# Kernel optimization log

Measured on AMD Instinct MI355X. Metric: run time of the kernel, lower is better.

## Reference

```python
import jax, jax.numpy as jnp
import numpy as np

B, C, H, W = 16, 384, 64, 64
S, R, GR = 16, 8, 64
EPS = 1e-6


def setup_inputs() -> dict:
    key = jax.random.key(0)
    ks = jax.random.split(key, 16)
    def rn(k, shape, s):
        return jax.random.normal(k, shape, dtype=jnp.float32) * s
    inp = {"x": jax.random.normal(ks[0], (B, C, H, W), dtype=jnp.float32)}
    i = 1
    for p in ("row", "col"):
        inp[p + "_a_logit"] = jnp.zeros((S,), jnp.float32)
        inp[p + "_U"] = rn(ks[i], (S, R), 0.02); i += 1
        inp[p + "_V"] = rn(ks[i], (S, R), 0.02); i += 1
        inp[p + "_Win"] = rn(ks[i], (S, C), 1.0 / np.sqrt(C)); i += 1
        inp[p + "_bin"] = jnp.zeros((S,), jnp.float32)
        inp[p + "_Wg"] = rn(ks[i], (S, C), 1.0 / np.sqrt(C)); i += 1
        inp[p + "_bg"] = jnp.zeros((S,), jnp.float32)
        inp[p + "_Wout"] = rn(ks[i], (C, S), 1.0 / np.sqrt(S)); i += 1
        inp[p + "_bout"] = jnp.zeros((C,), jnp.float32)
        inp[p + "_Wskip"] = rn(ks[i], (C, C), 1.0 / np.sqrt(C)); i += 1
        inp[p + "_bskip"] = jnp.zeros((C,), jnp.float32)
    inp["g1_w"] = rn(ks[i], (GR, C), 1.0 / np.sqrt(C)); i += 1
    inp["g1_b"] = jnp.zeros((GR,), jnp.float32)
    inp["g2_w"] = rn(ks[i], (C, GR), 1.0 / np.sqrt(GR)); i += 1
    inp["g2_b"] = jnp.zeros((C,), jnp.float32)
    inp["norm_w"] = jnp.ones((C,), jnp.float32)
    inp["norm_b"] = jnpp = jnp.zeros((C,), jnp.float32)
    inp["norm_b"] = jnp.zeros((C,), jnp.float32)
    return inp


def _ssm1d(x, a_logit, U, V, Win, bin_, Wg, bg, Wout, bout, Wskip, bskip, reverse):
    # x: [N, L, D]
    if reverse:
        x = x[:, ::-1]
    u = jnp.einsum('nld,sd->nls', x, Win) + bin_          # [N,L,S]
    g = jax.nn.sigmoid(jnp.einsum('nld,sd->nls', x, Wg) + bg)
    a = jax.nn.sigmoid(a_logit)                            # [S]
    # h_t = a*h + g_t*u_t + h @ (U V^T)^T  ==  h @ (diag(a) + (U V^T)^T) + g_t*u_t
    A = jnp.diag(a) + (U @ V.T).T                          # [S,S]
    gu = jnp.swapaxes(g * u, 0, 1)                         # [L,N,S]
    h0 = jnp.zeros((x.shape[0], a.shape[0]), x.dtype)

    def step(h, gu_t):
        h = h @ A + gu_t
        return h, h

    _, hs = jax.lax.scan(step, h0, gu)                     # [L,N,S]
    hs = jnp.swapaxes(hs, 0, 1)                            # [N,L,S]
    y = (jnp.einsum('nls,ds->nld', hs, Wout) + bout
         + jnp.einsum('nld,ed->nle', x, Wskip) + bskip)
    if reverse:
        y = y[:, ::-1]
    return y


def _forward(x, rp, cp, g1_w, g1_b, g2_w, g2_b, norm_w, norm_b):
    Bx, Cx, Hx, Wx = x.shape
    rows = jnp.transpose(x, (0, 2, 3, 1)).reshape(Bx * Hx, Wx, Cx)
    cols = jnp.transpose(x, (0, 3, 2, 1)).reshape(Bx * Wx, Hx, Cx)
    yr = _ssm1d(rows, *rp, False) + _ssm1d(rows, *rp, True)
    yc = _ssm1d(cols, *cp, False) + _ssm1d(cols, *cp, True)
    yr = jnp.transpose(yr.reshape(Bx, Hx, Wx, Cx), (0, 3, 1, 2))
    yc = jnp.transpose(yc.reshape(Bx, Wx, Hx, Cx), (0, 3, 2, 1))
    y = (yr + yc) * 0.25
    # LayerNorm over channel dim of BCHW
    mean = x.mean(axis=1, keepdims=True)
    var = ((x - mean) ** 2).mean(axis=1, keepdims=True)
    xn = (x - mean) / jnp.sqrt(var + EPS)
    xn = xn * norm_w[None, :, None, None] + norm_b[None, :, None, None]
    # gate: 1x1 conv -> GELU(exact) -> 1x1 conv -> sigmoid
    h1 = jax.nn.gelu(jnp.einsum('bchw,oc->bohw', xn, g1_w) + g1_b[None, :, None, None], approximate=False)
    g = jax.nn.sigmoid(jnp.einsum('bghw,cg->bchw', h1, g2_w) + g2_b[None, :, None, None])
    return g * y + (1.0 - g) * x


def reference(x, row_a_logit, row_U, row_V, row_Win, row_bin, row_Wg, row_bg, row_Wout, row_bout, row_Wskip, row_bskip, col_a_logit, col_U, col_V, col_Win, col_bin, col_Wg, col_bg, col_Wout, col_bout, col_Wskip, col_bskip, g1_w, g1_b, g2_w, g2_b, norm_w, norm_b):
    rp = (row_a_logit, row_U, row_V, row_Win, row_bin, row_Wg, row_bg, row_Wout, row_bout, row_Wskip, row_bskip)
    cp = (col_a_logit, col_U, col_V, col_Win, col_bin, col_Wg, col_bg, col_Wout, col_bout, col_Wskip, col_bskip)
    return _forward(x, rp, cp, g1_w, g1_b, g2_w, g2_b, norm_w, norm_b)
```

## Files before the change

kernel.cpp:

```cpp
#include <hip/hip_runtime.h>
#include <hip/hip_bf16.h>
#include <math.h>

#define PP 4096
#define CCH 384
#define NB 16

using short8 = __attribute__((ext_vector_type(8))) short;
using f32x4  = __attribute__((ext_vector_type(4))) float;
using half2t = __attribute__((ext_vector_type(2))) __fp16;

__device__ __forceinline__ float sigmoidf_(float v){ return 1.f/(1.f+expf(-v)); }
__device__ __forceinline__ float fast_sig(float v){
  return __builtin_amdgcn_rcpf(1.f + __builtin_amdgcn_exp2f(-v*1.44269504088896f));
}
__device__ __forceinline__ unsigned int f2bf(float f){
  __hip_bfloat16 h = __float2bfloat16(f);
  return (unsigned int)*reinterpret_cast<unsigned short*>(&h);
}
__device__ __forceinline__ float bf2f(unsigned short u){
  unsigned int w = ((unsigned int)u) << 16;
  return __uint_as_float(w);
}
__device__ __forceinline__ void gload_lds16(const void* g, void* l){
  __builtin_amdgcn_global_load_lds(
      (const __attribute__((address_space(1))) unsigned int*)g,
      (__attribute__((address_space(3))) unsigned int*)l, 16, 0, 0);
}

__global__ __launch_bounds__(256) void k_prep(
    const float* __restrict__ rAl, const float* __restrict__ rU, const float* __restrict__ rV,
    const float* __restrict__ cAl, const float* __restrict__ cU, const float* __restrict__ cV,
    const float* __restrict__ rWs, const float* __restrict__ cWs,
    const float* __restrict__ WinR, const float* __restrict__ WgR,
    const float* __restrict__ WinC, const float* __restrict__ WgC,
    const float* __restrict__ g1w, const float* __restrict__ nw, const float* __restrict__ nb,
    const float* __restrict__ g2w,
    const float* __restrict__ WoR, const float* __restrict__ WoC,
    float* __restrict__ Arow, float* __restrict__ Acol,
    unsigned short* __restrict__ WsumBf, unsigned short* __restrict__ WcatBf,
    unsigned short* __restrict__ g2wBf, unsigned short* __restrict__ WocatBf,
    float* __restrict__ t1, float* __restrict__ t2)
{
  int bid = blockIdx.x, tid = threadIdx.x;
  if (bid < 576) {
    int idx = bid*256 + tid;
    WsumBf[idx] = (unsigned short)f2bf(rWs[idx] + cWs[idx]);
  } else if (bid < 768) {
    int idx = (bid-576)*256 + tid;
    int row = idx / CCH, col = idx - row*CCH;
    float v;
    if      (row < 16)  v = WinR[row*CCH + col];
    else if (row < 32)  v = WgR [(row-16)*CCH + col];
    else if (row < 48)  v = WinC[(row-32)*CCH + col];
    else if (row < 64)  v = WgC [(row-48)*CCH + col];
    else                v = g1w[(row-64)*CCH + col]*nw[col];
    WcatBf[idx] = (unsigned short)f2bf(v);
  } else if (bid < 864) {
    int idx = (bid-768)*256 + tid;
    g2wBf[idx] = (unsigned short)f2bf(g2w[idx]);
  } else if (bid < 960) {
    int idx = (bid-864)*256 + tid;
    int c = idx >> 6, k = idx & 63;
    int sel = (k >> 4) & 1;
    float v = 0.5f * (sel ? WoC[c*16 + (k&15)] : WoR[c*16 + (k&15)]);
    WocatBf[idx] = (unsigned short)f2bf(v);
  } else {
    {
      int i = tid >> 4, j = tid & 15;
      float sr = 0.f, sc = 0.f;
      #pragma unroll
      for (int r=0;r<8;++r){ sr += rV[i*8+r]*rU[j*8+r]; sc += cV[i*8+r]*cU[j*8+r]; }
      if (i==j){ sr += sigmoidf_(rAl[i]); sc += sigmoidf_(cAl[i]); }
      Arow[tid] = sr; Acol[tid] = sc;
    }
    if (tid < 64) {
      float s1=0.f, s2=0.f;
      for (int c=0;c<CCH;++c){ s1 += g1w[tid*CCH+c]*nw[c]; s2 += nb[c]*g1w[tid*CCH+c]; }
      t1[tid]=s1; t2[tid]=s2;
    }
  }
}

__global__ __launch_bounds__(256) void k_xf(
    const float* __restrict__ x, const unsigned short* __restrict__ WcatBf,
    const float* __restrict__ binR, const float* __restrict__ bgR,
    const float* __restrict__ binC, const float* __restrict__ bgC,
    const float* __restrict__ t1, const float* __restrict__ t2,
    const float* __restrict__ g1b,
    unsigned short* __restrict__ xbf,
    float* __restrict__ ugr, float* __restrict__ ugc,
    unsigned short* __restrict__ h1bf)
{
  int b = blockIdx.x >> 6, pt = blockIdx.x & 63;
  int t = threadIdx.x;
  int w = t >> 6, l = t & 63;
  int lr = l & 15, kq = l >> 4, kb8 = kq*8;
  int pl = t & 63, g4 = w;

  __shared__ unsigned short xtb[64*64];
  __shared__ float red[512];
  __shared__ float meanS[64], invS[64];

  const float* xb = x + (size_t)b*CCH*PP + pt*64;
  f32x4 acc[2][4] = {};
  float sx = 0.f, sx2 = 0.f;

  float xv[16];
  #pragma unroll
  for (int j=0;j<16;++j) xv[j] = xb[(size_t)(g4*16 + j)*PP + pl];

  const unsigned short* wrow0 = WcatBf + (size_t)(w*32 + lr)*CCH + kb8;
  const unsigned short* wrow1 = wrow0 + 16*CCH;
  unsigned short* xgo = xbf + ((size_t)(b*PP + pt*64))*CCH;

  #pragma unroll
  for (int cc=0; cc<6; ++cc) {
    unsigned int pk[8];
    #pragma unroll
    for (int j=0;j<16;++j){ sx += xv[j]; sx2 += xv[j]*xv[j]; }
    #pragma unroll
    for (int j=0;j<8;++j) pk[j] = f2bf(xv[2*j]) | (f2bf(xv[2*j+1])<<16);
    __syncthreads();
    {
      int kg0 = g4*2, kg1 = g4*2+1;
      uint4 v0 = make_uint4(pk[0],pk[1],pk[2],pk[3]);
      uint4 v1 = make_uint4(pk[4],pk[5],pk[6],pk[7]);
      *(uint4*)&xtb[(size_t)(pl*8 + (kg0 ^ (pl&7)))*8] = v0;
      *(uint4*)&xtb[(size_t)(pl*8 + (kg1 ^ (pl&7)))*8] = v1;
    }
    if (cc < 5) {
      #pragma unroll
      for (int j=0;j<16;++j) xv[j] = xb[(size_t)((cc+1)*64 + g4*16 + j)*PP + pl];
    }
    short8 a0k0 = *(const short8*)(wrow0 + cc*64);
    short8 a0k1 = *(const short8*)(wrow0 + cc*64 + 32);
    short8 a1k0 = *(const short8*)(wrow1 + cc*64);
    short8 a1k1 = *(const short8*)(wrow1 + cc*64 + 32);
    __syncthreads();
    #pragma unroll
    for (int ks=0; ks<2; ++ks){
      int kg = ks*4 + kq;
      #pragma unroll
      for (int nf=0; nf<4; ++nf){
        int pr = nf*16 + lr;
        short8 bv = *(const short8*)&xtb[(size_t)(pr*8 + (kg ^ (pr&7)))*8];
        acc[0][nf] = __builtin_amdgcn_mfma_f32_16x16x32_bf16(ks? a0k1:a0k0, bv, acc[0][nf], 0,0,0);
        acc[1][nf] = __builtin_amdgcn_mfma_f32_16x16x32_bf16(ks? a1k1:a1k0, bv, acc[1][nf], 0,0,0);
      }
    }
    #pragma unroll
    for (int it=0; it<2; ++it){
      int p2 = 32*it + (t>>3), kg2 = t & 7;
      uint4 v = *(const uint4*)&xtb[(size_t)(p2*8 + (kg2 ^ (p2&7)))*8];
      *(uint4*)&xgo[(size_t)p2*CCH + cc*64 + kg2*8] = v;
    }
  }

  __syncthreads();
  red[g4*64 + pl] = sx;
  red[256 + g4*64 + pl] = sx2;
  __syncthreads();
  if (t < 64) {
    float s1 = red[t] + red[64+t] + red[128+t] + red[192+t];
    float s2 = red[256+t] + red[320+t] + red[384+t] + red[448+t];
    float mu = s1 * (1.f/CCH);
    float var = s2 * (1.f/CCH) - mu*mu;
    meanS[t] = mu;
    invS[t]  = rsqrtf(var + 1e-6f);
  }
  __syncthreads();

  if (w < 2) {
    const float* bu = w ? binC : binR;
    const float* bg = w ? bgC  : bgR;
    float* dst = w ? ugc : ugr;
    float bus[4], bgs[4];
    #pragma unroll
    for (int r=0;r<4;++r){ int s = kq*4 + r; bus[r]=bu[s]; bgs[r]=bg[s]; }
    #pragma unroll
    for (int nf=0; nf<4; ++nf){
      size_t pbase = ((size_t)(b*PP + pt*64 + nf*16 + lr))*16;
      #pragma unroll
      for (int r=0;r<4;++r){
        int s = kq*4 + r;
        float u = acc[0][nf][r] + bus[r];
        float g = fast_sig(acc[1][nf][r] + bgs[r]);
        dst[pbase + s] = u*g;
      }
    }
  } else {
    int ob = (w-2)*32 + kq*4;
    float t1o[2][4], t2o[2][4], gbo[2][4];
    #pragma unroll
    for (int mi=0;mi<2;++mi)
      #pragma unroll
      for (int r=0;r<4;++r){
        int o = ob + mi*16 + r;
        t1o[mi][r]=t1[o]; t2o[mi][r]=t2[o]; gbo[mi][r]=g1b[o];
      }
    #pragma unroll
    for (int nf=0; nf<4; ++nf){
      int pLoc = nf*16 + lr;
      float mu = meanS[pLoc], iv = invS[pLoc];
      #pragma unroll
      for (int mi=0;mi<2;++mi){
        unsigned int us[4];
        #pragma unroll
        for (int r=0;r<4;++r){
          float pre = iv*(acc[mi][nf][r] - mu*t1o[mi][r]) + t2o[mi][r] + gbo[mi][r];
          float ge = 0.5f*pre*(1.f + erff(pre*0.70710678118654752f));
          us[r] = f2bf(ge);
        }
        uint2 o2; o2.x = us[0] | (us[1]<<16); o2.y = us[2] | (us[3]<<16);
        *reinterpret_cast<uint2*>(h1bf + ((size_t)(b*PP + pt*64 + pLoc))*64 + (w-2)*32 + mi*16 + kq*4) = o2;
      }
    }
  }
}

__global__ __launch_bounds__(256) void k_scan(
    const float* __restrict__ ugr, const float* __restrict__ ugc,
    const float* __restrict__ Arow, const float* __restrict__ Acol,
    unsigned short* __restrict__ hs2)
{
  int W = blockIdx.x*4 + (threadIdx.x >> 6);
  int lane = threadIdx.x & 63;
  int tsk = W*4 + (lane >> 4);
  int s = lane & 15, base = lane & 48;
  int dir = tsk >> 11;
  int rem = tsk & 2047;
  int isCol = rem >> 10;
  int gg = rem & 1023;
  int b = gg >> 6, rc = gg & 63;
  const float* ug = isCol ? ugc : ugr;
  const float* A  = isCol ? Acol : Arow;
  int off = dir*32 + isCol*16;
  int p0 = b*PP + (isCol ? rc : rc*64);
  int stride = isCol ? 64 : 1;
  float ac[16];
  #pragma unroll
  for (int i=0;i<16;++i) ac[i] = A[i*16 + s];
  float h = 0.f;
  #pragma unroll 4
  for (int st=0; st<64; ++st){
    int l2 = dir ? (63-st) : st;
    float gu = ug[((size_t)(p0 + l2*stride))*16 + s];
    float tt = 0.f;
    #pragma unroll
    for (int i=0;i<16;++i) tt += __shfl(h, base + i, 64) * ac[i];
    h = tt + gu;
    hs2[((size_t)(p0 + l2*stride))*64 + off + s] = (unsigned short)f2bf(h);
  }
}

__global__ __launch_bounds__(512, 4) void k_fused(
    const unsigned short* __restrict__ xbf,
    const unsigned short* __restrict__ WsumBf,
    const unsigned short* __restrict__ h1bf, const unsigned short* __restrict__ g2wBf,
    const unsigned short* __restrict__ hs2, const unsigned short* __restrict__ WocatBf,
    const float* __restrict__ g2b,
    const float* __restrict__ boR, const float* __restrict__ bsR,
    const float* __restrict__ boC, const float* __restrict__ bsC,
    float* __restrict__ outp)
{
  int obid = blockIdx.x;
  int bid = ((obid & 7) * 128) + (obid >> 3);
  int b = bid >> 6, pt = bid & 63;
  int t = threadIdx.x;
  int w = t >> 6, l = t & 63;
  int lr = l & 15, kq = l >> 4, kb8 = kq * 8;
  int cw = w*48;

  __shared__ unsigned short xt[64*48*8];

  short8 gaw[3][2], gbv[2][4];
  {
    const unsigned short* hbase = h1bf + ((size_t)(b*PP + pt*64 + lr))*64 + kb8;
    #pragma unroll
    for (int ks=0; ks<2; ++ks)
      #pragma unroll
      for (int nf=0; nf<4; ++nf)
        gbv[ks][nf] = *(const short8*)(hbase + (size_t)nf*16*64 + ks*32);
    #pragma unroll
    for (int mi=0; mi<3; ++mi){
      const unsigned short* wbg = g2wBf + (size_t)(cw + mi*16 + lr)*64 + kb8;
      gaw[mi][0] = *(const short8*)(wbg);
      gaw[mi][1] = *(const short8*)(wbg + 32);
    }
  }

  {
    const unsigned short* xrow0 = xbf + ((size_t)(b*PP + pt*64))*CCH;
    #pragma unroll
    for (int i=0;i<6;++i){
      int G = w*384 + i*64 + l;
      int p = G/48, kgs = G - p*48;
      int kg = (kgs & ~7) | ((kgs & 7) ^ (p & 7));
      gload_lds16(xrow0 + (size_t)p*CCH + kg*8, &xt[(size_t)G*8]);
    }
  }

  unsigned int gt[3][4][2];
  {
    f32x4 gac[3][4] = {};
    #pragma unroll
    for (int ks=0; ks<2; ++ks)
      #pragma unroll
      for (int nf=0; nf<4; ++nf)
        #pragma unroll
        for (int mi=0; mi<3; ++mi)
          gac[mi][nf] = __builtin_amdgcn_mfma_f32_16x16x32_bf16(gaw[mi][ks], gbv[ks][nf], gac[mi][nf], 0,0,0);
    #pragma unroll
    for (int mi=0;mi<3;++mi){
      float4 gb4 = *(const float4*)&g2b[cw + mi*16 + kq*4];
      #pragma unroll
      for (int nf=0;nf<4;++nf){
        float s0 = fast_sig(gac[mi][nf][0] + gb4.x);
        float s1 = fast_sig(gac[mi][nf][1] + gb4.y);
        float s2 = fast_sig(gac[mi][nf][2] + gb4.z);
        float s3 = fast_sig(gac[mi][nf][3] + gb4.w);
        half2t p01 = __builtin_amdgcn_cvt_pkrtz(s0, s1);
        half2t p23 = __builtin_amdgcn_cvt_pkrtz(s2, s3);
        __builtin_memcpy(&gt[mi][nf][0], &p01, 4);
        __builtin_memcpy(&gt[mi][nf][1], &p23, 4);
      }
    }
  }

  __syncthreads();

  f32x4 acc[3][4] = {};
  const unsigned short* wbS = WsumBf + (size_t)(cw + lr)*CCH + kb8;
  #pragma unroll
  for (int c=0;c<6;++c){
    short8 a[3][2];
    #pragma unroll
    for (int mi=0;mi<3;++mi){
      a[mi][0] = *(const short8*)(wbS + (size_t)mi*16*CCH + c*64);
      a[mi][1] = *(const short8*)(wbS + (size_t)mi*16*CCH + c*64 + 32);
    }
    #pragma unroll
    for (int ks=0;ks<2;++ks){
      int kgl = ks*4 + kq;
      #pragma unroll
      for (int nf=0;nf<4;++nf){
        int pr = nf*16 + lr;
        int kgs = c*8 + (kgl ^ (pr & 7));
        short8 bv = *(const short8*)&xt[(size_t)(pr*48 + kgs)*8];
        #pragma unroll
        for (int mi=0;mi<3;++mi)
          acc[mi][nf] = __builtin_amdgcn_mfma_f32_16x16x32_bf16(a[mi][ks], bv, acc[mi][nf], 0,0,0);
      }
    }
  }

  {
    const unsigned short* hb2 = hs2 + ((size_t)(b*PP + pt*64 + lr))*64 + kb8;
    short8 hv[2][4];
    #pragma unroll
    for (int ks=0;ks<2;++ks)
      #pragma unroll
      for (int nf=0;nf<4;++nf)
        hv[ks][nf] = *(const short8*)(hb2 + (size_t)nf*16*64 + ks*32);
    #pragma unroll
    for (int mi=0;mi<3;++mi){
      const unsigned short* wo = WocatBf + (size_t)(cw + mi*16 + lr)*64 + kb8;
      short8 wa0 = *(const short8*)(wo);
      short8 wa1 = *(const short8*)(wo + 32);
      #pragma unroll
      for (int nf=0;nf<4;++nf){
        acc[mi][nf] = __builtin_amdgcn_mfma_f32_16x16x32_bf16(wa0, hv[0][nf], acc[mi][nf], 0,0,0);
        acc[mi][nf] = __builtin_amdgcn_mfma_f32_16x16x32_bf16(wa1, hv[1][nf], acc[mi][nf], 0,0,0);
      }
    }
  }

  #pragma unroll
  for (int mi=0;mi<3;++mi){
    int cb0 = cw + mi*16 + kq*4;
    float4 b1 = *(const float4*)&boR[cb0];
    float4 b2 = *(const float4*)&bsR[cb0];
    float4 b3 = *(const float4*)&boC[cb0];
    float4 b4 = *(const float4*)&bsC[cb0];
    float cb4[4] = { b1.x+b2.x+b3.x+b4.x, b1.y+b2.y+b3.y+b4.y,
                     b1.z+b2.z+b3.z+b4.z, b1.w+b2.w+b3.w+b4.w };
    int kgR = cb0 >> 3, eoff = cb0 & 7;
    #pragma unroll
    for (int nf=0;nf<4;++nf){
      int p = nf*16 + lr;
      int kgsR = (kgR & ~7) | ((kgR & 7) ^ (p & 7));
      uint2 xres = *(const uint2*)&xt[(size_t)(p*48 + kgsR)*8 + eoff];
      half2t g01, g23;
      __builtin_memcpy(&g01, &gt[mi][nf][0], 4);
      __builtin_memcpy(&g23, &gt[mi][nf][1], 4);
      float gv[4] = { (float)g01[0], (float)g01[1], (float)g23[0], (float)g23[1] };
      #pragma unroll
      for (int r=0;r<4;++r){
        unsigned int word = (r < 2) ? xres.x : xres.y;
        unsigned short us = (r & 1) ? (unsigned short)(word >> 16) : (unsigned short)(word & 0xffff);
        float xv = bf2f(us);
        float y = 0.5f*acc[mi][nf][r] + 0.5f*cb4[r];
        float gtv = gv[r];
        size_t addr = ((size_t)(b*CCH + cb0 + r))*PP + pt*64 + p;
        outp[addr] = gtv*y + (1.f-gtv)*xv;
      }
    }
  }
}

extern "C" void kernel_launch(void* const* d_in, const int* in_sizes, int n_in,
                              void* d_out, int out_size, void* d_ws, size_t ws_size,
                              hipStream_t stream)
{
  const float* x    = (const float*)d_in[0];
  const float* rAl  = (const float*)d_in[1];
  const float* rU   = (const float*)d_in[2];
  const float* rV   = (const float*)d_in[3];
  const float* rWin = (const float*)d_in[4];
  const float* rbin = (const float*)d_in[5];
  const float* rWg  = (const float*)d_in[6];
  const float* rbg  = (const float*)d_in[7];
  const float* rWo  = (const float*)d_in[8];
  const float* rbo  = (const float*)d_in[9];
  const float* rWs  = (const float*)d_in[10];
  const float* rbs  = (const float*)d_in[11];
  const float* cAl  = (const float*)d_in[12];
  const float* cU   = (const float*)d_in[13];
  const float* cV   = (const float*)d_in[14];
  const float* cWin = (const float*)d_in[15];
  const float* cbin = (const float*)d_in[16];
  const float* cWg  = (const float*)d_in[17];
  const float* cbg  = (const float*)d_in[18];
  const float* cWo  = (const float*)d_in[19];
  const float* cbo  = (const float*)d_in[20];
  const float* cWs  = (const float*)d_in[21];
  const float* cbs  = (const float*)d_in[22];
  const float* g1w  = (const float*)d_in[23];
  const float* g1b  = (const float*)d_in[24];
  const float* g2w  = (const float*)d_in[25];
  const float* g2b  = (const float*)d_in[26];
  const float* nw   = (const float*)d_in[27];
  const float* nb   = (const float*)d_in[28];

  float* ws   = (float*)d_ws;
  float* ugr  = ws;
  float* ugc  = ugr + 1048576;
  float* Arow = ugc + 1048576;
  float* Acol = Arow + 256;
  float* t1   = Acol + 256;
  float* t2   = t1 + 64;
  unsigned short* xbf     = (unsigned short*)(t2 + 64);
  unsigned short* h1bf    = xbf + (size_t)25165824;
  unsigned short* hs2     = h1bf + (size_t)4194304;
  unsigned short* WsumBf  = hs2 + (size_t)4194304;
  unsigned short* WcatBf  = WsumBf + 147456;
  unsigned short* g2wBf   = WcatBf + 49152;
  unsigned short* WocatBf = g2wBf + 24576;
  float* outp = (float*)d_out;

  k_prep<<<961, 256, 0, stream>>>(rAl,rU,rV,cAl,cU,cV,rWs,cWs,
                                  rWin,rWg,cWin,cWg,g1w,nw,nb,g2w,rWo,cWo,
                                  Arow,Acol,WsumBf,WcatBf,g2wBf,WocatBf,t1,t2);
  k_xf<<<1024, 256, 0, stream>>>(x, WcatBf, rbin, rbg, cbin, cbg,
                                 t1, t2, g1b, xbf, ugr, ugc, h1bf);
  k_scan<<<256, 256, 0, stream>>>(ugr, ugc, Arow, Acol, hs2);
  k_fused<<<1024, 512, 0, stream>>>(xbf, WsumBf, h1bf, g2wBf,
                                    hs2, WocatBf, g2b,
                                    rbo, rbs, cbo, cbs, outp);
}
```

Measured before the change: 153.8 us.

## Double-buffer k_xf LDS, tanh-GELU, split scan matvec, hoist hs2 loads

k_xf now double-buffers the transposed x tile in LDS, dropping one barrier per channel chunk and prefetching two chunks ahead. The exact erf GELU is replaced by the tanh approximation computed through a fast sigmoid, which changes numerics slightly. k_scan splits each 16-wide matvec across two half-groups joined by a shuffle-xor, launches twice as many blocks, and prefetches the next gu value. k_fused issues the hs2 fragment loads earlier so their latency overlaps the main GEMM.

Result: slower. 172.0 us (+11.8%).

```diff
diff --git a/kernel.cpp b/kernel.cpp
--- a/kernel.cpp
+++ b/kernel.cpp
@@ -98,7 +98,7 @@
   int lr = l & 15, kq = l >> 4, kb8 = kq*8;
   int pl = t & 63, g4 = w;
 
-  __shared__ unsigned short xtb[64*64];
+  __shared__ unsigned short xtb[2][64*64];
   __shared__ float red[512];
   __shared__ float meanS[64], invS[64];
 
@@ -106,45 +106,56 @@
   f32x4 acc[2][4] = {};
   float sx = 0.f, sx2 = 0.f;
 
-  float xv[16];
-  #pragma unroll
-  for (int j=0;j<16;++j) xv[j] = xb[(size_t)(g4*16 + j)*PP + pl];
-
   const unsigned short* wrow0 = WcatBf + (size_t)(w*32 + lr)*CCH + kb8;
   const unsigned short* wrow1 = wrow0 + 16*CCH;
   unsigned short* xgo = xbf + ((size_t)(b*PP + pt*64))*CCH;
 
+  float xv[16];
+  #pragma unroll
+  for (int j=0;j<16;++j) xv[j] = xb[(size_t)(g4*16 + j)*PP + pl];
+
+  {
+    unsigned int pk[8];
+    #pragma unroll
+    for (int j=0;j<16;++j){ sx += xv[j]; sx2 += xv[j]*xv[j]; }
+    #pragma unroll
+    for (int j=0;j<8;++j) pk[j] = f2bf(xv[2*j]) | (f2bf(xv[2*j+1])<<16);
+    int kg0 = g4*2, kg1 = g4*2+1;
+    *(uint4*)&xtb[0][(size_t)(pl*8 + (kg0 ^ (pl&7)))*8] = make_uint4(pk[0],pk[1],pk[2],pk[3]);
+    *(uint4*)&xtb[0][(size_t)(pl*8 + (kg1 ^ (pl&7)))*8] = make_uint4(pk[4],pk[5],pk[6],pk[7]);
+  }
+  #pragma unroll
+  for (int j=0;j<16;++j) xv[j] = xb[(size_t)(64 + g4*16 + j)*PP + pl];
+  __syncthreads();
+
   #pragma unroll
   for (int cc=0; cc<6; ++cc) {
-    unsigned int pk[8];
-    #pragma unroll
-    for (int j=0;j<16;++j){ sx += xv[j]; sx2 += xv[j]*xv[j]; }
-    #pragma unroll
-    for (int j=0;j<8;++j) pk[j] = f2bf(xv[2*j]) | (f2bf(xv[2*j+1])<<16);
-    __syncthreads();
-    {
+    int cur = cc & 1;
+    if (cc < 5) {
+      unsigned int pk[8];
+      #pragma unroll
+      for (int j=0;j<16;++j){ sx += xv[j]; sx2 += xv[j]*xv[j]; }
+      #pragma unroll
+      for (int j=0;j<8;++j) pk[j] = f2bf(xv[2*j]) | (f2bf(xv[2*j+1])<<16);
       int kg0 = g4*2, kg1 = g4*2+1;
-      uint4 v0 = make_uint4(pk[0],pk[1],pk[2],pk[3]);
-      uint4 v1 = make_uint4(pk[4],pk[5],pk[6],pk[7]);
-      *(uint4*)&xtb[(size_t)(pl*8 + (kg0 ^ (pl&7)))*8] = v0;
-      *(uint4*)&xtb[(size_t)(pl*8 + (kg1 ^ (pl&7)))*8] = v1;
-    }
-    if (cc < 5) {
-      #pragma unroll
-      for (int j=0;j<16;++j) xv[j] = xb[(size_t)((cc+1)*64 + g4*16 + j)*PP + pl];
+      *(uint4*)&xtb[cur^1][(size_t)(pl*8 + (kg0 ^ (pl&7)))*8] = make_uint4(pk[0],pk[1],pk[2],pk[3]);
+      *(uint4*)&xtb[cur^1][(size_t)(pl*8 + (kg1 ^ (pl&7)))*8] = make_uint4(pk[4],pk[5],pk[6],pk[7]);
+      if (cc < 4) {
+        #pragma unroll
+        for (int j=0;j<16;++j) xv[j] = xb[(size_t)((cc+2)*64 + g4*16 + j)*PP + pl];
+      }
     }
     short8 a0k0 = *(const short8*)(wrow0 + cc*64);
     short8 a0k1 = *(const short8*)(wrow0 + cc*64 + 32);
     short8 a1k0 = *(const short8*)(wrow1 + cc*64);
     short8 a1k1 = *(const short8*)(wrow1 + cc*64 + 32);
-    __syncthreads();
     #pragma unroll
     for (int ks=0; ks<2; ++ks){
       int kg = ks*4 + kq;
       #pragma unroll
       for (int nf=0; nf<4; ++nf){
         int pr = nf*16 + lr;
-        short8 bv = *(const short8*)&xtb[(size_t)(pr*8 + (kg ^ (pr&7)))*8];
+        short8 bv = *(const short8*)&xtb[cur][(size_t)(pr*8 + (kg ^ (pr&7)))*8];
         acc[0][nf] = __builtin_amdgcn_mfma_f32_16x16x32_bf16(ks? a0k1:a0k0, bv, acc[0][nf], 0,0,0);
         acc[1][nf] = __builtin_amdgcn_mfma_f32_16x16x32_bf16(ks? a1k1:a1k0, bv, acc[1][nf], 0,0,0);
       }
@@ -152,12 +163,12 @@
     #pragma unroll
     for (int it=0; it<2; ++it){
       int p2 = 32*it + (t>>3), kg2 = t & 7;
-      uint4 v = *(const uint4*)&xtb[(size_t)(p2*8 + (kg2 ^ (p2&7)))*8];
+      uint4 v = *(const uint4*)&xtb[cur][(size_t)(p2*8 + (kg2 ^ (p2&7)))*8];
       *(uint4*)&xgo[(size_t)p2*CCH + cc*64 + kg2*8] = v;
     }
-  }
-
-  __syncthreads();
+    __syncthreads();
+  }
+
   red[g4*64 + pl] = sx;
   red[256 + g4*64 + pl] = sx2;
   __syncthreads();
@@ -209,7 +220,8 @@
         #pragma unroll
         for (int r=0;r<4;++r){
           float pre = iv*(acc[mi][nf][r] - mu*t1o[mi][r]) + t2o[mi][r] + gbo[mi][r];
-          float ge = 0.5f*pre*(1.f + erff(pre*0.70710678118654752f));
+          float aa = pre*(1.f + 0.044715f*pre*pre);
+          float ge = pre*fast_sig(1.5957691216f*aa);
           us[r] = f2bf(ge);
         }
         uint2 o2; o2.x = us[0] | (us[1]<<16); o2.y = us[2] | (us[3]<<16);
@@ -224,10 +236,11 @@
     const float* __restrict__ Arow, const float* __restrict__ Acol,
     unsigned short* __restrict__ hs2)
 {
-  int W = blockIdx.x*4 + (threadIdx.x >> 6);
+  int Wv = blockIdx.x*4 + (threadIdx.x >> 6);
   int lane = threadIdx.x & 63;
-  int tsk = W*4 + (lane >> 4);
-  int s = lane & 15, base = lane & 48;
+  int tsk = Wv*2 + (lane >> 5);
+  int base32 = lane & 32;
+  int half = (lane >> 4) & 1, s = lane & 15;
   int dir = tsk >> 11;
   int rem = tsk & 2047;
   int isCol = rem >> 10;
@@ -238,19 +251,28 @@
   int off = dir*32 + isCol*16;
   int p0 = b*PP + (isCol ? rc : rc*64);
   int stride = isCol ? 64 : 1;
-  float ac[16];
-  #pragma unroll
-  for (int i=0;i<16;++i) ac[i] = A[i*16 + s];
+  float ac[8];
+  #pragma unroll
+  for (int i=0;i<8;++i) ac[i] = A[(half*8 + i)*16 + s];
   float h = 0.f;
+  int l2_0 = dir ? 63 : 0;
+  float gu = ug[((size_t)(p0 + l2_0*stride))*16 + s];
   #pragma unroll 4
   for (int st=0; st<64; ++st){
     int l2 = dir ? (63-st) : st;
-    float gu = ug[((size_t)(p0 + l2*stride))*16 + s];
-    float tt = 0.f;
-    #pragma unroll
-    for (int i=0;i<16;++i) tt += __shfl(h, base + i, 64) * ac[i];
+    float gu_next = 0.f;
+    if (st < 63){
+      int l2n = dir ? (62-st) : (st+1);
+      gu_next = ug[((size_t)(p0 + l2n*stride))*16 + s];
+    }
+    float part = 0.f;
+    #pragma unroll
+    for (int i=0;i<8;++i) part += __shfl(h, base32 + half*8 + i, 64) * ac[i];
+    float tt = part + __shfl_xor(part, 16, 64);
     h = tt + gu;
-    hs2[((size_t)(p0 + l2*stride))*64 + off + s] = (unsigned short)f2bf(h);
+    if (!(lane & 16))
+      hs2[((size_t)(p0 + l2*stride))*64 + off + s] = (unsigned short)f2bf(h);
+    gu = gu_next;
   }
 }
 
@@ -289,6 +311,15 @@
       gaw[mi][1] = *(const short8*)(wbg + 32);
     }
   }
+  short8 hv[2][4];
+  {
+    const unsigned short* hb2 = hs2 + ((size_t)(b*PP + pt*64 + lr))*64 + kb8;
+    #pragma unroll
+    for (int ks=0;ks<2;++ks)
+      #pragma unroll
+      for (int nf=0;nf<4;++nf)
+        hv[ks][nf] = *(const short8*)(hb2 + (size_t)nf*16*64 + ks*32);
+  }
 
   {
     const unsigned short* xrow0 = xbf + ((size_t)(b*PP + pt*64))*CCH;
@@ -356,13 +387,6 @@
   }
 
   {
-    const unsigned short* hb2 = hs2 + ((size_t)(b*PP + pt*64 + lr))*64 + kb8;
-    short8 hv[2][4];
-    #pragma unroll
-    for (int ks=0;ks<2;++ks)
-      #pragma unroll
-      for (int nf=0;nf<4;++nf)
-        hv[ks][nf] = *(const short8*)(hb2 + (size_t)nf*16*64 + ks*32);
     #pragma unroll
     for (int mi=0;mi<3;++mi){
       const unsigned short* wo = WocatBf + (size_t)(cw + mi*16 + lr)*64 + kb8;
@@ -464,7 +488,7 @@
                                   Arow,Acol,WsumBf,WcatBf,g2wBf,WocatBf,t1,t2);
   k_xf<<<1024, 256, 0, stream>>>(x, WcatBf, rbin, rbg, cbin, cbg,
                                  t1, t2, g1b, xbf, ugr, ugc, h1bf);
-  k_scan<<<256, 256, 0, stream>>>(ugr, ugc, Arow, Acol, hs2);
+  k_scan<<<512, 256, 0, stream>>>(ugr, ugc, Arow, Acol, hs2);
   k_fused<<<1024, 512, 0, stream>>>(xbf, WsumBf, h1bf, g2wBf,
                                     hs2, WocatBf, g2b,
                                     rbo, rbs, cbo, cbs, outp);
```
